# Kernel tuning notes

Measured on AMD Instinct MI355X. Metric: run time of the kernel, lower is better.

## Reference

```python
import jax, jax.numpy as jnp
import numpy as np

B, H, S, D = 4, 16, 2048, 64

def setup_inputs() -> dict:
    key = jax.random.key(0)
    kq, kk, kv = jax.random.split(key, 3)
    q = jax.random.normal(kq, (B, H, S, D), dtype=jnp.float32)
    k = jax.random.normal(kk, (B, H, S, D), dtype=jnp.float32)
    v = jax.random.normal(kv, (B, H, S, D), dtype=jnp.float32)
    return {"q": q, "k": k, "v": v}

def reference(q, k, v):
    # Faithful port of TransformerBlock.scaled_dot_product_attention
    # (is_causal=True, mha_dropout=0.0 / eval mode).
    head_dim = q.shape[-1]
    scale = jnp.asarray(head_dim, q.dtype) ** -0.5
    q_len, k_len = q.shape[-2], k.shape[-2]
    # causal additive bias: 0 on/below diagonal, -inf above
    causal = jnp.tril(jnp.ones((q_len, k_len), dtype=bool))
    attn_bias = jnp.where(causal, jnp.asarray(0.0, q.dtype), jnp.asarray(-jnp.inf, q.dtype))
    # [b,h,s,d] x [b,h,t,d] -> [b,h,s,t]
    attn_weights = jnp.einsum('bhsd,bhtd->bhst', q * scale, k) + attn_bias
    attn = jax.nn.softmax(attn_weights, axis=-1)
    out = jnp.einsum('bhst,bhtd->bhsd', attn, v)
    return out
```

## Files before the change

kernel.cpp:

```cpp
#include <hip/hip_runtime.h>
#include <math.h>


#define S_LEN 2048
#define D_DIM 64
#define TK 64
#define NHEAD 64
#define MNEG -30000.0f
#define DEFER_THR 12.0f
#define LSTR 72
#define PREP_KBLK 4096

typedef __attribute__((ext_vector_type(8))) short bf16x8;
typedef __attribute__((ext_vector_type(4))) float f32x4;

static __device__ __forceinline__ float fast_exp2(float x) {
#if __has_builtin(__builtin_amdgcn_exp2f)
    return __builtin_amdgcn_exp2f(x);
#else
    float r;
    asm volatile("v_exp_f32 %0, %1\n\ts_nop 1" : "=v"(r) : "v"(x));
    return r;
#endif
}

static __device__ __forceinline__ float fmax3(float a, float b, float c) {
    return fmaxf(fmaxf(a, b), c);
}

static __device__ __forceinline__ unsigned int pack_bf16(float a, float b) {
    union { float f; unsigned int u; } ca, cb;
    ca.f = a; cb.f = b;
    unsigned int ua = ca.u + 0x8000u;
    unsigned int ub = cb.u + 0x8000u;
    return (ua >> 16) | (ub & 0xFFFF0000u);
}

typedef const __attribute__((address_space(1))) unsigned int* gas1_t;
typedef __attribute__((address_space(3))) unsigned int* las3_t;
static __device__ __forceinline__ void stage16(const void* g, void* l) {
    __builtin_amdgcn_global_load_lds((gas1_t)g, (las3_t)l, 16, 0, 0);
}

__global__ __launch_bounds__(256)
void fa_prep(const float* __restrict__ kg, const float* __restrict__ vg,
             unsigned short* __restrict__ kb, unsigned short* __restrict__ vb)
{
    const int tid = threadIdx.x;
    const int bid = blockIdx.x;
    if (bid < PREP_KBLK) {
        const int cid = bid * 256 + tid;
        const int ch  = cid & 7;
        const int row = cid >> 3;
        const int kv  = row & (S_LEN - 1);
        const float4* s = reinterpret_cast<const float4*>(kg + (size_t)row * D_DIM + ch * 8);
        float4 a = s[0], b = s[1];
        uint4 w;
        w.x = pack_bf16(a.x, a.y); w.y = pack_bf16(a.z, a.w);
        w.z = pack_bf16(b.x, b.y); w.w = pack_bf16(b.z, b.w);
        const int dst = ch ^ (kv & 7);
        *reinterpret_cast<uint4*>(kb + (size_t)row * D_DIM + dst * 8) = w;
    } else {
        const int wv   = (bid - PREP_KBLK) * 4 + (tid >> 6);
        const int lane = tid & 63;
        const int kg8  = lane >> 3;
        const int dg   = lane & 7;
        const float* s = vg + ((size_t)wv * TK + kg8 * 8) * D_DIM + dg * 8;
        float va[8][8];
        #pragma unroll
        for (int i = 0; i < 8; ++i) {
            const float4* sp = reinterpret_cast<const float4*>(s + (size_t)i * D_DIM);
            float4 x = sp[0], y = sp[1];
            va[i][0] = x.x; va[i][1] = x.y; va[i][2] = x.z; va[i][3] = x.w;
            va[i][4] = y.x; va[i][5] = y.y; va[i][6] = y.z; va[i][7] = y.w;
        }
        unsigned short* db = vb + (size_t)wv * (TK * D_DIM);
        #pragma unroll
        for (int j = 0; j < 8; ++j) {
            const int d = dg * 8 + j;
            uint4 w;
            w.x = pack_bf16(va[0][j], va[1][j]);
            w.y = pack_bf16(va[2][j], va[3][j]);
            w.z = pack_bf16(va[4][j], va[5][j]);
            w.w = pack_bf16(va[6][j], va[7][j]);
            *reinterpret_cast<uint4*>(db + d * D_DIM + 8 * (kg8 ^ j)) = w;
        }
    }
}

__global__ __launch_bounds__(256, 4)
void fa_fwd(const float* __restrict__ qg,
            const unsigned short* __restrict__ kb,
            const unsigned short* __restrict__ vb,
            float* __restrict__ og)
{
    const int head = blockIdx.x;
    const int pr   = blockIdx.y;
    const int tid  = threadIdx.x;
    const int wave = tid >> 6;
    const int lane = tid & 63;
    const int m16  = lane & 15;
    const int quad = lane >> 4;

    __shared__ unsigned short Kl[2][TK * D_DIM];
    __shared__ unsigned short Vt[2][TK * D_DIM];
    __shared__ unsigned short Pl[4][16 * TK];

    const size_t hoff = (size_t)head * S_LEN * D_DIM;
    const unsigned short* kbh = kb + hoff;
    const unsigned short* vbh = vb + hoff;
    float* __restrict__ ogh = og + hoff;

    const int swz  = (m16 & 7) << 4;
    const int colA = (quad * 16) ^ swz;
    const int colB = (64 + quad * 16) ^ swz;
    const int rowB = m16 * 128;
    const int sgo  = wave * 512 + lane * 8;

    char* klds = (char*)&Kl[0][0];
    char* vlds = (char*)&Vt[0][0];
    char* plds = (char*)&Pl[0][0] + wave * 2048 + m16 * 128;
    char* kw   = klds + wave * 1024;
    char* vw   = vlds + wave * 1024;

    const float QSC = 0.18033688011112042f;

    for (int pass = 0; pass < 2; ++pass) {
        const int q0 = ((pass == 0) ? pr : (31 - pr)) * TK;
        const int T  = q0 >> 6;

        bf16x8 qf[2];
        {
            const float* qp = qg + hoff + (size_t)(q0 + wave * 16 + m16) * D_DIM + quad * 8;
            #pragma unroll
            for (int c = 0; c < 2; ++c) {
                float4 a = reinterpret_cast<const float4*>(qp + c * 32)[0];
                float4 b = reinterpret_cast<const float4*>(qp + c * 32)[1];
                unsigned int u0 = pack_bf16(a.x * QSC, a.y * QSC);
                unsigned int u1 = pack_bf16(a.z * QSC, a.w * QSC);
                unsigned int u2 = pack_bf16(b.x * QSC, b.y * QSC);
                unsigned int u3 = pack_bf16(b.z * QSC, b.w * QSC);
                qf[c][0] = (short)(u0 & 0xFFFF); qf[c][1] = (short)(u0 >> 16);
                qf[c][2] = (short)(u1 & 0xFFFF); qf[c][3] = (short)(u1 >> 16);
                qf[c][4] = (short)(u2 & 0xFFFF); qf[c][5] = (short)(u2 >> 16);
                qf[c][6] = (short)(u3 & 0xFFFF); qf[c][7] = (short)(u3 >> 16);
            }
        }

        float m_i = MNEG, l_i = 0.f;
        f32x4 oacc[4];
        #pragma unroll
        for (int nc = 0; nc < 4; ++nc) oacc[nc] = (f32x4){0.f, 0.f, 0.f, 0.f};

        {
            const unsigned short* ks = kbh + sgo;
            const unsigned short* vs = vbh + sgo;
            stage16(ks,        kw);
            stage16(ks + 2048, kw + 4096);
            stage16(vs,        vw);
            stage16(vs + 2048, vw + 4096);
        }
        __syncthreads();

        int cur = 0;
        for (int t = 0; t <= T; ++t) {
            if (t < T) {
                const unsigned short* ks = kbh + (size_t)(t + 1) * 4096 + sgo;
                const unsigned short* vs = vbh + (size_t)(t + 1) * 4096 + sgo;
                const int nb = (cur ^ 1) * 8192;
                stage16(ks,        kw + nb);
                stage16(ks + 2048, kw + nb + 4096);
                stage16(vs,        vw + nb);
                stage16(vs + 2048, vw + nb + 4096);
            }

            const char* kt = klds + cur * 8192;
            const char* vt = vlds + cur * 8192;

            float sv[4][4];
            #pragma unroll
            for (int nt = 0; nt < 4; ++nt) {
                f32x4 acc = (f32x4){0.f, 0.f, 0.f, 0.f};
                const char* kr = kt + nt * 2048 + rowB;
                bf16x8 kf0 = *reinterpret_cast<const bf16x8*>(kr + colA);
                bf16x8 kf1 = *reinterpret_cast<const bf16x8*>(kr + colB);
                acc = __builtin_amdgcn_mfma_f32_16x16x32_bf16(kf0, qf[0], acc, 0, 0, 0);
                acc = __builtin_amdgcn_mfma_f32_16x16x32_bf16(kf1, qf[1], acc, 0, 0, 0);
                #pragma unroll
                for (int r = 0; r < 4; ++r) sv[nt][r] = acc[r];
            }

            if (t == T) {
                #pragma unroll
                for (int nt = 0; nt < 4; ++nt)
                    #pragma unroll
                    for (int r = 0; r < 4; ++r)
                        if (nt * 16 + quad * 4 + r > wave * 16 + m16) sv[nt][r] = MNEG;
            }

            float t0 = fmax3(sv[0][0], sv[0][1], sv[0][2]);
            float t1 = fmax3(sv[0][3], sv[1][0], sv[1][1]);
            float t2 = fmax3(sv[1][2], sv[1][3], sv[2][0]);
            float t3 = fmax3(sv[2][1], sv[2][2], sv[2][3]);
            float t4 = fmax3(sv[3][0], sv[3][1], sv[3][2]);
            float u0 = fmax3(t0, t1, t2);
            float u1 = fmax3(t3, t4, sv[3][3]);
            float rm = fmaxf(u0, u1);
            rm = fmaxf(rm, __shfl_xor(rm, 16, 64));
            rm = fmaxf(rm, __shfl_xor(rm, 32, 64));

            if (__any(rm > m_i + DEFER_THR)) {
                float mnew  = fmaxf(m_i, rm);
                float alpha = fast_exp2(m_i - mnew);
                l_i *= alpha;
                #pragma unroll
                for (int nc = 0; nc < 4; ++nc)
                    #pragma unroll
                    for (int r = 0; r < 4; ++r) oacc[nc][r] *= alpha;
                m_i = mnew;
            }

            float rs = 0.f;
            #pragma unroll
            for (int nt = 0; nt < 4; ++nt) {
                float e0 = fast_exp2(sv[nt][0] - m_i);
                float e1 = fast_exp2(sv[nt][1] - m_i);
                float e2 = fast_exp2(sv[nt][2] - m_i);
                float e3 = fast_exp2(sv[nt][3] - m_i);
                rs += (e0 + e1) + (e2 + e3);
                uint2 pw;
                pw.x = pack_bf16(e0, e1);
                pw.y = pack_bf16(e2, e3);
                *reinterpret_cast<uint2*>(plds + ((nt * 32 + quad * 8) ^ swz)) = pw;
            }
            rs += __shfl_xor(rs, 16, 64);
            rs += __shfl_xor(rs, 32, 64);
            l_i += rs;

            asm volatile("s_waitcnt lgkmcnt(0)" ::: "memory");

            bf16x8 pf0 = *reinterpret_cast<const bf16x8*>(plds + colA);
            bf16x8 pf1 = *reinterpret_cast<const bf16x8*>(plds + colB);
            #pragma unroll
            for (int nc = 0; nc < 4; ++nc) {
                const char* vr = vt + nc * 2048 + rowB;
                bf16x8 vf0 = *reinterpret_cast<const bf16x8*>(vr + colA);
                bf16x8 vf1 = *reinterpret_cast<const bf16x8*>(vr + colB);
                oacc[nc] = __builtin_amdgcn_mfma_f32_16x16x32_bf16(vf0, pf0, oacc[nc], 0, 0, 0);
                oacc[nc] = __builtin_amdgcn_mfma_f32_16x16x32_bf16(vf1, pf1, oacc[nc], 0, 0, 0);
            }

            __syncthreads();
            cur ^= 1;
        }

        float inv = 1.0f / l_i;
        float* op = ogh + (size_t)(q0 + wave * 16 + m16) * D_DIM;
        #pragma unroll
        for (int nc = 0; nc < 4; ++nc) {
            float4 o4;
            o4.x = oacc[nc][0] * inv;
            o4.y = oacc[nc][1] * inv;
            o4.z = oacc[nc][2] * inv;
            o4.w = oacc[nc][3] * inv;
            reinterpret_cast<float4*>(op + nc * 16 + quad * 4)[0] = o4;
        }
    }
}

__global__ __launch_bounds__(256, 4)
void fa_fwd_fb(const float* __restrict__ qg,
               const float* __restrict__ kg,
               const float* __restrict__ vg,
               float* __restrict__ og)
{
    const int head = blockIdx.x;
    const int pr   = blockIdx.y;
    const int tid  = threadIdx.x;
    const int wave = tid >> 6;
    const int lane = tid & 63;
    const int m16  = lane & 15;
    const int quad = lane >> 4;

    __shared__ unsigned short Kl[TK][LSTR];
    __shared__ unsigned short Vt[D_DIM][LSTR];
    __shared__ unsigned short Pl[4][16][LSTR];

    const size_t hoff = (size_t)head * S_LEN * D_DIM;
    const float* kh = kg + hoff;
    const float* vh = vg + hoff;

    const int ksr = tid >> 2;
    const int ksc = (tid & 3) << 4;
    const int va  = lane >> 3;
    const int vb  = lane & 7;
    const int vrr = wave * 16 + 2 * vb;
    const int vcc = 8 * va;
    const float LOG2E = 1.4426950408889634f;

    for (int pass = 0; pass < 2; ++pass) {
        const int q0 = ((pass == 0) ? pr : (31 - pr)) * TK;

        bf16x8 qf[2];
        {
            const float* qp = qg + hoff + (size_t)(q0 + wave * 16 + m16) * D_DIM + quad * 8;
            #pragma unroll
            for (int c = 0; c < 2; ++c) {
                float4 a = reinterpret_cast<const float4*>(qp + c * 32)[0];
                float4 b = reinterpret_cast<const float4*>(qp + c * 32)[1];
                unsigned int u0 = pack_bf16(a.x * 0.125f, a.y * 0.125f);
                unsigned int u1 = pack_bf16(a.z * 0.125f, a.w * 0.125f);
                unsigned int u2 = pack_bf16(b.x * 0.125f, b.y * 0.125f);
                unsigned int u3 = pack_bf16(b.z * 0.125f, b.w * 0.125f);
                qf[c][0] = (short)(u0 & 0xFFFF); qf[c][1] = (short)(u0 >> 16);
                qf[c][2] = (short)(u1 & 0xFFFF); qf[c][3] = (short)(u1 >> 16);
                qf[c][4] = (short)(u2 & 0xFFFF); qf[c][5] = (short)(u2 >> 16);
                qf[c][6] = (short)(u3 & 0xFFFF); qf[c][7] = (short)(u3 >> 16);
            }
        }

        float m_i = MNEG, l_i = 0.f;
        f32x4 oacc[4];
        #pragma unroll
        for (int nc = 0; nc < 4; ++nc) oacc[nc] = (f32x4){0.f, 0.f, 0.f, 0.f};

        float4 kA, kB, kC, kD, vA, vB, vC, vD;
        {
            const float* kp = kh + (size_t)ksr * D_DIM + ksc;
            kA = reinterpret_cast<const float4*>(kp)[0];
            kB = reinterpret_cast<const float4*>(kp)[1];
            kC = reinterpret_cast<const float4*>(kp)[2];
            kD = reinterpret_cast<const float4*>(kp)[3];
            const float* vp = vh + (size_t)vrr * D_DIM + vcc;
            vA = reinterpret_cast<const float4*>(vp)[0];
            vB = reinterpret_cast<const float4*>(vp)[1];
            vC = reinterpret_cast<const float4*>(vp + D_DIM)[0];
            vD = reinterpret_cast<const float4*>(vp + D_DIM)[1];
        }

        for (int j0 = 0; j0 <= q0; j0 += TK) {
            __syncthreads();
            {
                uint4 w0, w1;
                w0.x = pack_bf16(kA.x, kA.y); w0.y = pack_bf16(kA.z, kA.w);
                w0.z = pack_bf16(kB.x, kB.y); w0.w = pack_bf16(kB.z, kB.w);
                w1.x = pack_bf16(kC.x, kC.y); w1.y = pack_bf16(kC.z, kC.w);
                w1.z = pack_bf16(kD.x, kD.y); w1.w = pack_bf16(kD.z, kD.w);
                *reinterpret_cast<uint4*>(&Kl[ksr][ksc])     = w0;
                *reinterpret_cast<uint4*>(&Kl[ksr][ksc + 8]) = w1;

                float r0[8] = {vA.x, vA.y, vA.z, vA.w, vB.x, vB.y, vB.z, vB.w};
                float r1[8] = {vC.x, vC.y, vC.z, vC.w, vD.x, vD.y, vD.z, vD.w};
                #pragma unroll
                for (int jj = 0; jj < 8; ++jj) {
                    int j = (jj + va) & 7;
                    *reinterpret_cast<unsigned int*>(&Vt[vcc + j][vrr]) = pack_bf16(r0[j], r1[j]);
                }
            }
            __syncthreads();

            if (j0 + TK <= q0) {
                const float* kp = kh + (size_t)(j0 + TK + ksr) * D_DIM + ksc;
                kA = reinterpret_cast<const float4*>(kp)[0];
                kB = reinterpret_cast<const float4*>(kp)[1];
                kC = reinterpret_cast<const float4*>(kp)[2];
                kD = reinterpret_cast<const float4*>(kp)[3];
                const float* vp = vh + (size_t)(j0 + TK + vrr) * D_DIM + vcc;
                vA = reinterpret_cast<const float4*>(vp)[0];
                vB = reinterpret_cast<const float4*>(vp)[1];
                vC = reinterpret_cast<const float4*>(vp + D_DIM)[0];
                vD = reinterpret_cast<const float4*>(vp + D_DIM)[1];
            }

            float sv[4][4];
            #pragma unroll
            for (int nt = 0; nt < 4; ++nt) {
                f32x4 acc = (f32x4){0.f, 0.f, 0.f, 0.f};
                bf16x8 kf0 = *reinterpret_cast<const bf16x8*>(&Kl[nt * 16 + m16][quad * 8]);
                bf16x8 kf1 = *reinterpret_cast<const bf16x8*>(&Kl[nt * 16 + m16][32 + quad * 8]);
                acc = __builtin_amdgcn_mfma_f32_16x16x32_bf16(kf0, qf[0], acc, 0, 0, 0);
                acc = __builtin_amdgcn_mfma_f32_16x16x32_bf16(kf1, qf[1], acc, 0, 0, 0);
                #pragma unroll
                for (int r = 0; r < 4; ++r) sv[nt][r] = acc[r];
            }

            if (j0 == q0) {
                #pragma unroll
                for (int nt = 0; nt < 4; ++nt)
                    #pragma unroll
                    for (int r = 0; r < 4; ++r)
                        if (nt * 16 + quad * 4 + r > wave * 16 + m16) sv[nt][r] = MNEG;
            }

            float a0 = fmaxf(fmaxf(sv[0][0], sv[0][1]), fmaxf(sv[0][2], sv[0][3]));
            float a1 = fmaxf(fmaxf(sv[1][0], sv[1][1]), fmaxf(sv[1][2], sv[1][3]));
            float a2 = fmaxf(fmaxf(sv[2][0], sv[2][1]), fmaxf(sv[2][2], sv[2][3]));
            float a3 = fmaxf(fmaxf(sv[3][0], sv[3][1]), fmaxf(sv[3][2], sv[3][3]));
            float rm = fmaxf(fmaxf(a0, a1), fmaxf(a2, a3));
            rm = fmaxf(rm, __shfl_xor(rm, 16, 64));
            rm = fmaxf(rm, __shfl_xor(rm, 32, 64));
            float mnew  = fmaxf(m_i, rm);
            float alpha = fast_exp2((m_i - mnew) * LOG2E);
            float msc   = mnew * LOG2E;
            m_i = mnew;

            float rs = 0.f;
            #pragma unroll
            for (int nt = 0; nt < 4; ++nt) {
                float e0 = fast_exp2(fmaf(sv[nt][0], LOG2E, -msc));
                float e1 = fast_exp2(fmaf(sv[nt][1], LOG2E, -msc));
                float e2 = fast_exp2(fmaf(sv[nt][2], LOG2E, -msc));
                float e3 = fast_exp2(fmaf(sv[nt][3], LOG2E, -msc));
                rs += (e0 + e1) + (e2 + e3);
                uint2 pw;
                pw.x = pack_bf16(e0, e1);
                pw.y = pack_bf16(e2, e3);
                *reinterpret_cast<uint2*>(&Pl[wave][m16][nt * 16 + quad * 4]) = pw;
            }
            rs += __shfl_xor(rs, 16, 64);
            rs += __shfl_xor(rs, 32, 64);
            l_i = fmaf(alpha, l_i, rs);

            #pragma unroll
            for (int nc = 0; nc < 4; ++nc)
                #pragma unroll
                for (int r = 0; r < 4; ++r)
                    oacc[nc][r] *= alpha;

            asm volatile("s_waitcnt lgkmcnt(0)" ::: "memory");

            bf16x8 pf0 = *reinterpret_cast<const bf16x8*>(&Pl[wave][m16][quad * 8]);
            bf16x8 pf1 = *reinterpret_cast<const bf16x8*>(&Pl[wave][m16][32 + quad * 8]);
            #pragma unroll
            for (int nc = 0; nc < 4; ++nc) {
                bf16x8 vf0 = *reinterpret_cast<const bf16x8*>(&Vt[nc * 16 + m16][quad * 8]);
                bf16x8 vf1 = *reinterpret_cast<const bf16x8*>(&Vt[nc * 16 + m16][32 + quad * 8]);
                oacc[nc] = __builtin_amdgcn_mfma_f32_16x16x32_bf16(vf0, pf0, oacc[nc], 0, 0, 0);
                oacc[nc] = __builtin_amdgcn_mfma_f32_16x16x32_bf16(vf1, pf1, oacc[nc], 0, 0, 0);
            }
        }

        float inv = 1.0f / l_i;
        float* op = og + hoff + (size_t)(q0 + wave * 16 + m16) * D_DIM;
        #pragma unroll
        for (int nc = 0; nc < 4; ++nc) {
            float4 o4;
            o4.x = oacc[nc][0] * inv;
            o4.y = oacc[nc][1] * inv;
            o4.z = oacc[nc][2] * inv;
            o4.w = oacc[nc][3] * inv;
            reinterpret_cast<float4*>(op + nc * 16 + quad * 4)[0] = o4;
        }
    }
}

extern "C" void kernel_launch(void* const* d_in, const int* in_sizes, int n_in,
                              void* d_out, int out_size, void* d_ws, size_t ws_size,
                              hipStream_t stream) {
    const float* q = (const float*)d_in[0];
    const float* k = (const float*)d_in[1];
    const float* v = (const float*)d_in[2];
    float* o = (float*)d_out;
    const size_t kvShorts = (size_t)NHEAD * S_LEN * D_DIM;
    const size_t wsNeed   = 2 * kvShorts * sizeof(unsigned short);
    dim3 grid(NHEAD, 16);
    if (d_ws != nullptr && ws_size >= wsNeed) {
        unsigned short* kb = (unsigned short*)d_ws;
        unsigned short* vb = kb + kvShorts;
        fa_prep<<<PREP_KBLK + 512, 256, 0, stream>>>(k, v, kb, vb);
        fa_fwd<<<grid, 256, 0, stream>>>(q, kb, vb, o);
    } else {
        fa_fwd_fb<<<grid, 256, 0, stream>>>(q, k, v, o);
    }
}
```

Baseline: 206.9 us.

## Fold running max into MFMA accumulator init, add setprio and perm-based bf16 pack

The running max is now carried as a negative bias in the accumulator initial value of the QK MFMA, so the scores come out already shifted and the per-element subtraction before exp2 goes away. On a rescale, the scores and the bias are shifted by the new max. The change also wraps both MFMA phases in s_setprio to favour matrix-issuing waves, and packs to bf16 with a single v_perm instead of shift/mask. The initial bias of 1000 and the altered rescale condition add numerical risk, but rescales should stay rare.

After: 201.0 us. 1.03x faster.

```diff
diff --git a/kernel.cpp b/kernel.cpp
--- a/kernel.cpp
+++ b/kernel.cpp
@@ -6,8 +6,10 @@
 #define D_DIM 64
 #define TK 64
 #define NHEAD 64
+#define MASKV -30000.0f
+#define MINIT 1000.0f
+#define DEFER_THR 12.0f
 #define MNEG -30000.0f
-#define DEFER_THR 12.0f
 #define LSTR 72
 #define PREP_KBLK 4096
 
@@ -34,6 +36,16 @@
     unsigned int ua = ca.u + 0x8000u;
     unsigned int ub = cb.u + 0x8000u;
     return (ua >> 16) | (ub & 0xFFFF0000u);
+}
+
+static __device__ __forceinline__ unsigned int pack_bf16_fast(float a, float b) {
+#if __has_builtin(__builtin_amdgcn_perm)
+    union { float f; unsigned int u; } ca, cb;
+    ca.f = a; cb.f = b;
+    return __builtin_amdgcn_perm(cb.u + 0x8000u, ca.u + 0x8000u, 0x07060302u);
+#else
+    return pack_bf16(a, b);
+#endif
 }
 
 typedef const __attribute__((address_space(1))) unsigned int* gas1_t;
@@ -147,7 +159,8 @@
             }
         }
 
-        float m_i = MNEG, l_i = 0.f;
+        float l_i = 0.f;
+        f32x4 mc = (f32x4){MINIT, MINIT, MINIT, MINIT};
         f32x4 oacc[4];
         #pragma unroll
         for (int nc = 0; nc < 4; ++nc) oacc[nc] = (f32x4){0.f, 0.f, 0.f, 0.f};
@@ -178,24 +191,25 @@
             const char* vt = vlds + cur * 8192;
 
             float sv[4][4];
+            __builtin_amdgcn_s_setprio(1);
             #pragma unroll
             for (int nt = 0; nt < 4; ++nt) {
-                f32x4 acc = (f32x4){0.f, 0.f, 0.f, 0.f};
                 const char* kr = kt + nt * 2048 + rowB;
                 bf16x8 kf0 = *reinterpret_cast<const bf16x8*>(kr + colA);
                 bf16x8 kf1 = *reinterpret_cast<const bf16x8*>(kr + colB);
-                acc = __builtin_amdgcn_mfma_f32_16x16x32_bf16(kf0, qf[0], acc, 0, 0, 0);
+                f32x4 acc = __builtin_amdgcn_mfma_f32_16x16x32_bf16(kf0, qf[0], mc, 0, 0, 0);
                 acc = __builtin_amdgcn_mfma_f32_16x16x32_bf16(kf1, qf[1], acc, 0, 0, 0);
                 #pragma unroll
                 for (int r = 0; r < 4; ++r) sv[nt][r] = acc[r];
             }
+            __builtin_amdgcn_s_setprio(0);
 
             if (t == T) {
                 #pragma unroll
                 for (int nt = 0; nt < 4; ++nt)
                     #pragma unroll
                     for (int r = 0; r < 4; ++r)
-                        if (nt * 16 + quad * 4 + r > wave * 16 + m16) sv[nt][r] = MNEG;
+                        if (nt * 16 + quad * 4 + r > wave * 16 + m16) sv[nt][r] = MASKV;
             }
 
             float t0 = fmax3(sv[0][0], sv[0][1], sv[0][2]);
@@ -209,28 +223,33 @@
             rm = fmaxf(rm, __shfl_xor(rm, 16, 64));
             rm = fmaxf(rm, __shfl_xor(rm, 32, 64));
 
-            if (__any(rm > m_i + DEFER_THR)) {
-                float mnew  = fmaxf(m_i, rm);
-                float alpha = fast_exp2(m_i - mnew);
+            if (__any(rm > DEFER_THR)) {
+                float mx    = fmaxf(rm, 0.f);
+                float alpha = fast_exp2(-mx);
                 l_i *= alpha;
                 #pragma unroll
                 for (int nc = 0; nc < 4; ++nc)
                     #pragma unroll
                     for (int r = 0; r < 4; ++r) oacc[nc][r] *= alpha;
-                m_i = mnew;
+                #pragma unroll
+                for (int nt = 0; nt < 4; ++nt)
+                    #pragma unroll
+                    for (int r = 0; r < 4; ++r) sv[nt][r] -= mx;
+                #pragma unroll
+                for (int r = 0; r < 4; ++r) mc[r] -= mx;
             }
 
             float rs = 0.f;
             #pragma unroll
             for (int nt = 0; nt < 4; ++nt) {
-                float e0 = fast_exp2(sv[nt][0] - m_i);
-                float e1 = fast_exp2(sv[nt][1] - m_i);
-                float e2 = fast_exp2(sv[nt][2] - m_i);
-                float e3 = fast_exp2(sv[nt][3] - m_i);
+                float e0 = fast_exp2(sv[nt][0]);
+                float e1 = fast_exp2(sv[nt][1]);
+                float e2 = fast_exp2(sv[nt][2]);
+                float e3 = fast_exp2(sv[nt][3]);
                 rs += (e0 + e1) + (e2 + e3);
                 uint2 pw;
-                pw.x = pack_bf16(e0, e1);
-                pw.y = pack_bf16(e2, e3);
+                pw.x = pack_bf16_fast(e0, e1);
+                pw.y = pack_bf16_fast(e2, e3);
                 *reinterpret_cast<uint2*>(plds + ((nt * 32 + quad * 8) ^ swz)) = pw;
             }
             rs += __shfl_xor(rs, 16, 64);
@@ -241,6 +260,7 @@
 
             bf16x8 pf0 = *reinterpret_cast<const bf16x8*>(plds + colA);
             bf16x8 pf1 = *reinterpret_cast<const bf16x8*>(plds + colB);
+            __builtin_amdgcn_s_setprio(1);
             #pragma unroll
             for (int nc = 0; nc < 4; ++nc) {
                 const char* vr = vt + nc * 2048 + rowB;
@@ -249,6 +269,7 @@
                 oacc[nc] = __builtin_amdgcn_mfma_f32_16x16x32_bf16(vf0, pf0, oacc[nc], 0, 0, 0);
                 oacc[nc] = __builtin_amdgcn_mfma_f32_16x16x32_bf16(vf1, pf1, oacc[nc], 0, 0, 0);
             }
+            __builtin_amdgcn_s_setprio(0);
 
             __syncthreads();
             cur ^= 1;
```
